# Kernel optimization log

Measured on AMD Instinct MI355X. Metric: run time of the kernel, lower is better.

The kernel has to match this reference:

```python
import jax, jax.numpy as jnp
import numpy as np

B, C, H, W = 4, 512, 64, 64
D = 512  # model_dim


def setup_inputs() -> dict:
    key = jax.random.key(0)
    ks = jax.random.split(key, 9)
    s = 0.02
    return {
        "q": jax.random.normal(ks[0], (B, C, H, W), dtype=jnp.float32),
        "Wq": jax.random.normal(ks[1], (D, C), dtype=jnp.float32) * s,
        "bq": jax.random.normal(ks[2], (D,), dtype=jnp.float32) * s,
        "Wk": jax.random.normal(ks[3], (D, C), dtype=jnp.float32) * s,
        "bk": jax.random.normal(ks[4], (D,), dtype=jnp.float32) * s,
        "Wv": jax.random.normal(ks[5], (D, C), dtype=jnp.float32) * s,
        "bv": jax.random.normal(ks[6], (D,), dtype=jnp.float32) * s,
        "Wo": jax.random.normal(ks[7], (C, D), dtype=jnp.float32) * s,
        "bo": jax.random.normal(ks[8], (C,), dtype=jnp.float32) * s,
    }


def reference(q, Wq, bq, Wk, bk, Wv, bv, Wo, bo):
    b, c, h, w = q.shape
    # 1x1 conv == per-pixel linear over channels; tokens s = h*w
    x = q.reshape(b, c, h * w)                      # (b, c, s)
    Q = jnp.einsum('bcs,dc->bsd', x, Wq) + bq       # (b, s, D)
    K = jnp.einsum('bcs,dc->bsd', x, Wk) + bk
    V = jnp.einsum('bcs,dc->bsd', x, Wv) + bv
    # ScaleAttend: scale = q.shape[-1]^-0.5 = model_dim^-0.5 (heads not split)
    scale = jnp.asarray(Q.shape[-1], Q.dtype) ** -0.5
    sim = jnp.einsum('bsd,btd->bst', Q, K) * scale  # (b, s, s)
    attn = jax.nn.softmax(sim, axis=-1)
    o = jnp.einsum('bst,btd->bsd', attn, V)         # (b, s, D)
    # to_out 1x1 conv: D -> C
    y = jnp.einsum('bsd,cd->bsc', o, Wo) + bo       # (b, s, C)
    return y.transpose(0, 2, 1).reshape(b, c, h, w)
```

## Files before the change

### kernel.cpp

```cpp
#include <hip/hip_runtime.h>
#include <hip/hip_bf16.h>

typedef __hip_bfloat16 bf16;
typedef __attribute__((ext_vector_type(8))) short short8;
typedef __attribute__((ext_vector_type(4))) float floatx4;
typedef __attribute__((ext_vector_type(4))) short shortx4;

static constexpr int BATCH = 4;
static constexpr int CH    = 512;
static constexpr int SEQ   = 4096;
static constexpr int DM    = 512;

__device__ __forceinline__ void gload16(const void* g, void* l) {
  __builtin_amdgcn_global_load_lds(
      (const __attribute__((address_space(1))) unsigned int*)g,
      (__attribute__((address_space(3))) unsigned int*)l,
      16, 0, 0);
}

__device__ __forceinline__ float hw_exp2(float x) {
  float r;
  asm("v_exp_f32 %0, %1" : "=v"(r) : "v"(x));
  return r;
}

__global__ __launch_bounds__(256) void cvt_weights(
    const float* __restrict__ w0, const float* __restrict__ w1,
    const float* __restrict__ w2, const float* __restrict__ w3,
    bf16* __restrict__ out) {
  const float* src = (blockIdx.y == 0) ? w0 : (blockIdx.y == 1) ? w1
                   : (blockIdx.y == 2) ? w2 : w3;
  int idx = blockIdx.x * 256 + threadIdx.x;
  out[(long)blockIdx.y * (DM * CH) + idx] = __float2bfloat16(src[idx]);
}

__global__ __launch_bounds__(256) void transpose_cvt(
    const float* __restrict__ x, bf16* __restrict__ xT) {
  __shared__ float tile[64][65];
  const int s0 = blockIdx.x * 64, c0 = blockIdx.y * 64;
  const float* xb = x + (long)blockIdx.z * CH * SEQ;
  bf16* xTb = xT + (long)blockIdx.z * SEQ * CH;
  const int t = threadIdx.x;
  const int sl = t & 63, cq = t >> 6;
  #pragma unroll
  for (int i = 0; i < 16; ++i) {
    int cl = cq * 16 + i;
    tile[cl][sl] = xb[(long)(c0 + cl) * SEQ + s0 + sl];
  }
  __syncthreads();
  const int cl2 = t & 63, sq = t >> 6;
  #pragma unroll
  for (int i = 0; i < 16; ++i) {
    int sl2 = sq * 16 + i;
    xTb[(long)(s0 + sl2) * CH + c0 + cl2] = __float2bfloat16(tile[cl2][sl2]);
  }
}

template <int KIND>
__global__ __launch_bounds__(256, 2) void proj128(
    const bf16* __restrict__ A0, const bf16* __restrict__ Wbase,
    const float* __restrict__ b0, const float* __restrict__ b1,
    const float* __restrict__ b2, void* __restrict__ Cbase) {
  __shared__ __align__(16) bf16 As[2][128 * 64];
  __shared__ __align__(16) bf16 Bs[2][128 * 64];

  int id = blockIdx.x + gridDim.x * (blockIdx.y + gridDim.y * blockIdx.z);
  int nwg = gridDim.x * gridDim.y * gridDim.z;
  int sid = ((nwg & 7) == 0) ? ((id & 7) * (nwg >> 3) + (id >> 3)) : id;
  const int bx = sid % gridDim.x;
  const int by = (sid / gridDim.x) % gridDim.y;
  const int z  = sid / (gridDim.x * gridDim.y);
  const int mat = (KIND == 0) ? (z >> 2) : 0;
  const int bz  = (KIND == 0) ? (z & 3) : z;

  const long XSZ = (long)SEQ * CH;
  const long lK = CH;
  const bf16* Ab = A0 + (long)bz * XSZ + (long)by * 128 * lK;
  const bf16* Bb = Wbase + (long)mat * ((long)DM * CH) + (long)bx * 128 * lK;
  const float* bias = (KIND == 1) ? b0 : (mat == 0 ? b0 : mat == 1 ? b1 : b2);

  const int tid = threadIdx.x;
  const int w = tid >> 6, lane = tid & 63;
  const int wr = w >> 1, wc = w & 1;
  const int l16 = lane & 15, quad = lane >> 4;
  const int srow = tid >> 3;
  const int sp = tid & 7;
  const int slog = (sp ^ (srow & 7)) << 3;
  const int pA0 = (quad ^ (l16 & 7)) << 3;
  const int pA1 = pA0 ^ 32;

  auto stageA = [&](int buf, int kt) {
    const bf16* s = Ab + kt * 64 + (long)srow * lK + slog;
    char* d = (char*)(&As[buf][0]) + tid * 16;
    #pragma unroll
    for (int r = 0; r < 4; ++r)
      gload16(s + (long)(r * 32) * lK, d + r * 4096);
  };
  auto stageB = [&](int buf, int kt) {
    const bf16* s = Bb + kt * 64 + (long)srow * lK + slog;
    char* d = (char*)(&Bs[buf][0]) + tid * 16;
    #pragma unroll
    for (int r = 0; r < 4; ++r)
      gload16(s + (long)(r * 32) * lK, d + r * 4096);
  };

  floatx4 acc[4][4];
  #pragma unroll
  for (int m = 0; m < 4; ++m)
    #pragma unroll
    for (int n = 0; n < 4; ++n) acc[m][n] = (floatx4)(0.0f);

  const int nk = CH >> 6;
  stageA(0, 0); stageB(0, 0);
  __syncthreads();

  for (int t = 0; t < nk; ++t) {
    const int cur = t & 1, nxt = cur ^ 1;
    const bool more = (t + 1 < nk);
    #pragma unroll
    for (int kc = 0; kc < 2; ++kc) {
      const int poff = kc ? pA1 : pA0;
      short8 a[4], b[4];
      #pragma unroll
      for (int i = 0; i < 4; ++i)
        a[i] = *(const short8*)(&As[cur][0] + (wr * 64 + i * 16 + l16) * 64 + poff);
      #pragma unroll
      for (int j = 0; j < 4; ++j)
        b[j] = *(const short8*)(&Bs[cur][0] + (wc * 64 + j * 16 + l16) * 64 + poff);
      if (more) {
        if (kc == 0) stageA(nxt, t + 1);
        else         stageB(nxt, t + 1);
      }
      __builtin_amdgcn_s_setprio(1);
      #pragma unroll
      for (int i = 0; i < 4; ++i)
        #pragma unroll
        for (int j = 0; j < 4; ++j)
          acc[i][j] = __builtin_amdgcn_mfma_f32_16x16x32_bf16(
              a[i], b[j], acc[i][j], 0, 0, 0);
      __builtin_amdgcn_s_setprio(0);
    }
    __syncthreads();
  }

  const int rbase = by * 128 + wr * 64 + quad * 4;
  const int cbase = bx * 128 + wc * 64 + l16;
  #pragma unroll
  for (int m = 0; m < 4; ++m) {
    const int row = rbase + m * 16;
    #pragma unroll
    for (int n = 0; n < 4; ++n) {
      const int col = cbase + n * 16;
      floatx4 v = acc[m][n];
      const float bb = bias[col];
      if constexpr (KIND == 0) {
        if (mat < 2) {
          bf16* C = (bf16*)Cbase + (long)mat * (BATCH * XSZ) + (long)bz * XSZ;
          #pragma unroll
          for (int r = 0; r < 4; ++r)
            C[(long)(row + r) * DM + col] = __float2bfloat16(v[r] + bb);
        } else {
          bf16* C = (bf16*)Cbase + 2 * (BATCH * XSZ) + (long)bz * XSZ;
          alignas(8) bf16 tmp[4];
          #pragma unroll
          for (int r = 0; r < 4; ++r) tmp[r] = __float2bfloat16(v[r] + bb);
          *(shortx4*)(C + (long)col * SEQ + row) = *(const shortx4*)tmp;
        }
      } else {
        float* C = (float*)Cbase + (long)bz * XSZ;
        floatx4 o_;
        #pragma unroll
        for (int r = 0; r < 4; ++r) o_[r] = v[r] + bb;
        *(floatx4*)(C + (long)col * SEQ + row) = o_;
      }
    }
  }
}

__global__ __launch_bounds__(512, 2) void gemm_qk(
    const bf16* __restrict__ A, long sAz,
    const bf16* __restrict__ B, long sBz,
    bf16* __restrict__ C, long sCz,
    float scale, int K, int ldc) {
  __shared__ __align__(16) bf16 As[2][256 * 64];
  __shared__ __align__(16) bf16 Bs[2][256 * 64];

  int id = blockIdx.x + gridDim.x * (blockIdx.y + gridDim.y * blockIdx.z);
  int nwg = gridDim.x * gridDim.y * gridDim.z;
  int sid = ((nwg & 7) == 0) ? ((id & 7) * (nwg >> 3) + (id >> 3)) : id;
  const int bx = sid % gridDim.x;
  const int by = (sid / gridDim.x) % gridDim.y;
  const int bz = sid / (gridDim.x * gridDim.y);

  const int tid = threadIdx.x;
  const long lK = K;
  const bf16* Ab = A + (long)bz * sAz + (long)by * 256 * lK;
  const bf16* Bb = B + (long)bz * sBz + (long)bx * 256 * lK;

  const int w = tid >> 6, lane = tid & 63;
  const int wr = w >> 2, wc = w & 3;
  const int l16 = lane & 15, quad = lane >> 4;

  const int srow = tid >> 3;
  const int sp = tid & 7;
  const int slog = (sp ^ (srow & 7)) << 3;

  const int pA0 = (quad ^ (l16 & 7)) << 3;
  const int pA1 = pA0 ^ 32;

  auto stage_half = [&](const bf16* Gb, bf16* Lb, int kt, int h) {
    #pragma unroll
    for (int r = 0; r < 2; ++r) {
      const int row = h * 128 + r * 64 + srow;
      gload16(Gb + (long)kt * 64 + (long)row * lK + slog,
              (char*)Lb + row * 128 + sp * 16);
    }
  };

  floatx4 acc[8][4];
  #pragma unroll
  for (int m = 0; m < 8; ++m)
    #pragma unroll
    for (int n = 0; n < 4; ++n) acc[m][n] = (floatx4)(0.0f);

  const int nk = K >> 6;
  stage_half(Ab, &As[0][0], 0, 0); stage_half(Bb, &Bs[0][0], 0, 0);
  stage_half(Ab, &As[0][0], 0, 1); stage_half(Bb, &Bs[0][0], 0, 1);
  if (nk > 1) { stage_half(Ab, &As[1][0], 1, 0); stage_half(Bb, &Bs[1][0], 1, 0); }
  asm volatile("s_waitcnt vmcnt(4)" ::: "memory");
  __builtin_amdgcn_s_barrier();

  for (int tt = 0; tt < nk; tt += 2) {
    #pragma unroll
    for (int u = 0; u < 2; ++u) {
      const bf16* __restrict__ Al = &As[u][0];
      const bf16* __restrict__ Bl = &Bs[u][0];
      short8 a[2][4], b[2][2][2];
      #pragma unroll
      for (int p = 0; p < 4; ++p) {
        const int rm = p >> 1, cn = p & 1;
        if (cn == 0) {
          #pragma unroll
          for (int kc = 0; kc < 2; ++kc)
            #pragma unroll
            for (int i = 0; i < 4; ++i)
              a[kc][i] = *(const short8*)(
                  Al + (rm * 128 + wr * 64 + i * 16 + l16) * 64
                     + (kc ? pA1 : pA0));
        }
        if (rm == 0) {
          #pragma unroll
          for (int kc = 0; kc < 2; ++kc)
            #pragma unroll
            for (int j = 0; j < 2; ++j)
              b[kc][cn][j] = *(const short8*)(
                  Bl + (cn * 128 + wc * 32 + j * 16 + l16) * 64
                     + (kc ? pA1 : pA0));
        }
        {
          const int g = u * 4 + p;
          const int stile = tt + 1 + ((g + 2) >> 2);
          if (stile < nk) {
            const int sh = (p < 2) ? 1 : 0;
            if (p & 1) stage_half(Bb, &Bs[stile & 1][0], stile, sh);
            else       stage_half(Ab, &As[stile & 1][0], stile, sh);
          }
        }
        __builtin_amdgcn_sched_barrier(0);
        __builtin_amdgcn_s_barrier();
        asm volatile("s_waitcnt lgkmcnt(0)" ::: "memory");
        __builtin_amdgcn_sched_barrier(0);
        __builtin_amdgcn_s_setprio(1);
        #pragma unroll
        for (int kc = 0; kc < 2; ++kc)
          #pragma unroll
          for (int i = 0; i < 4; ++i)
            #pragma unroll
            for (int j = 0; j < 2; ++j)
              acc[rm * 4 + i][cn * 2 + j] =
                  __builtin_amdgcn_mfma_f32_16x16x32_bf16(
                      a[kc][i], b[kc][cn][j], acc[rm * 4 + i][cn * 2 + j],
                      0, 0, 0);
        __builtin_amdgcn_s_setprio(0);
        if (p == 3) {
          if (u == 0) {
            if (tt + 2 < nk) asm volatile("s_waitcnt vmcnt(4)" ::: "memory");
            else             asm volatile("s_waitcnt vmcnt(0)" ::: "memory");
          } else {
            if (tt + 2 < nk) asm volatile("s_waitcnt vmcnt(4)" ::: "memory");
          }
        }
        __builtin_amdgcn_s_barrier();
      }
    }
  }

  bf16* Cb = C + (long)bz * sCz;
  #pragma unroll
  for (int rm = 0; rm < 2; ++rm)
    #pragma unroll
    for (int i = 0; i < 4; ++i) {
      const int row = by * 256 + rm * 128 + wr * 64 + i * 16 + quad * 4;
      #pragma unroll
      for (int cn = 0; cn < 2; ++cn)
        #pragma unroll
        for (int j = 0; j < 2; ++j) {
          const int col = bx * 256 + cn * 128 + wc * 32 + j * 16 + l16;
          floatx4 v = acc[rm * 4 + i][cn * 2 + j];
          #pragma unroll
          for (int r = 0; r < 4; ++r)
            Cb[(long)(row + r) * ldc + col] = __float2bfloat16(v[r] * scale);
        }
    }
}

__global__ __launch_bounds__(512, 2) void fused_smpv(
    const bf16* __restrict__ Sim, const bf16* __restrict__ Vt,
    bf16* __restrict__ Ob) {
  __shared__ __align__(16) bf16 Apv[2][64 * 64];
  __shared__ float rl_lds[64];

  const int id = blockIdx.x + (blockIdx.y << 6);
  const int xcd = id & 7;
  const int bz = xcd >> 1;
  const int by = ((id >> 3) << 1) | (id & 1);

  const int tid = threadIdx.x;
  const bf16* Simb = Sim + (long)bz * ((long)SEQ * SEQ) + (long)(by * 64) * SEQ;
  const bf16* Vb   = Vt  + (long)bz * ((long)SEQ * CH);
  bf16* Obb        = Ob  + (long)bz * ((long)SEQ * CH) + (long)(by * 64) * CH;

  const int srow = tid >> 3;
  const int sp = tid & 7;
  const int aswz = (sp ^ (srow & 7)) << 4;

  const int w = tid >> 6, lane = tid & 63;
  const int l16 = lane & 15, quad = lane >> 4;
  const int pA0 = (quad ^ (l16 & 7)) << 3;
  const int pA1 = pA0 ^ 32;

  const bf16* Vw = Vb + (long)(w * 64 + l16) * SEQ + quad * 8;

  float lsum = 0.f;

  auto writeA = [&](int buf, uint4 u) {
    const ushort* h = (const ushort*)&u;
    union { uint4 u4; ushort hh[8]; } pk;
    #pragma unroll
    for (int k2 = 0; k2 < 8; ++k2) {
      float f = __uint_as_float(((unsigned)h[k2]) << 16);
      float e = hw_exp2(f);
      lsum += e;
      __hip_bfloat16 pb = __float2bfloat16(e);
      pk.hh[k2] = *(const ushort*)&pb;
    }
    *(uint4*)((char*)(&Apv[buf][0]) + srow * 128 + aswz) = pk.u4;
  };

  {
    uint4 ua = *(const uint4*)(Simb + (long)srow * SEQ + sp * 8);
    writeA(0, ua);
  }
  __syncthreads();

  floatx4 acc[4][4];
  #pragma unroll
  for (int i = 0; i < 4; ++i)
    #pragma unroll
    for (int j = 0; j < 4; ++j) acc[i][j] = (floatx4)(0.0f);

  const int nk = SEQ >> 6;
  for (int t = 0; t < nk; ++t) {
    const int cur = t & 1, nxt = cur ^ 1;
    const bool more = (t + 1 < nk);
    short8 b[2][4];
    #pragma unroll
    for (int j = 0; j < 4; ++j) {
      const bf16* p = Vw + (long)(j * 16) * SEQ + t * 64;
      b[0][j] = *(const short8*)(p);
      b[1][j] = *(const short8*)(p + 32);
    }
    uint4 un;
    if (more)
      un = *(const uint4*)(Simb + (long)srow * SEQ + (t + 1) * 64 + sp * 8);
    short8 a[2][4];
    #pragma unroll
    for (int kc = 0; kc < 2; ++kc) {
      const int poff = kc ? pA1 : pA0;
      #pragma unroll
      for (int i = 0; i < 4; ++i)
        a[kc][i] = *(const short8*)(&Apv[cur][0] + (i * 16 + l16) * 64 + poff);
    }
    __builtin_amdgcn_s_setprio(1);
    #pragma unroll
    for (int kc = 0; kc < 2; ++kc)
      #pragma unroll
      for (int i = 0; i < 4; ++i)
        #pragma unroll
        for (int j = 0; j < 4; ++j)
          acc[i][j] = __builtin_amdgcn_mfma_f32_16x16x32_bf16(
              a[kc][i], b[kc][j], acc[i][j], 0, 0, 0);
    __builtin_amdgcn_s_setprio(0);
    if (more) writeA(nxt, un);
    __syncthreads();
  }

  #pragma unroll
  for (int o = 1; o < 8; o <<= 1) lsum += __shfl_xor(lsum, o);
  if (sp == 0) rl_lds[srow] = 1.0f / lsum;
  __syncthreads();

  #pragma unroll
  for (int i = 0; i < 4; ++i) {
    #pragma unroll
    for (int j = 0; j < 4; ++j) {
      floatx4 v = acc[i][j];
      const int col = w * 64 + j * 16 + l16;
      #pragma unroll
      for (int r = 0; r < 4; ++r) {
        const int row = i * 16 + quad * 4 + r;
        Obb[(long)row * CH + col] = __float2bfloat16(v[r] * rl_lds[row]);
      }
    }
  }
}

extern "C" void kernel_launch(void* const* d_in, const int* in_sizes, int n_in,
                              void* d_out, int out_size, void* d_ws,
                              size_t ws_size, hipStream_t stream) {
  const float* q  = (const float*)d_in[0];
  const float* Wq = (const float*)d_in[1];
  const float* bq = (const float*)d_in[2];
  const float* Wk = (const float*)d_in[3];
  const float* bk = (const float*)d_in[4];
  const float* Wv = (const float*)d_in[5];
  const float* bv = (const float*)d_in[6];
  const float* Wo = (const float*)d_in[7];
  const float* bo = (const float*)d_in[8];
  float* out = (float*)d_out;

  bf16* ws = (bf16*)d_ws;
  const long WSZ = (long)DM * CH;
  const long XSZ = (long)SEQ * CH;
  const long SSZ = (long)SEQ * SEQ;
  bf16* Wqb = ws;
  bf16* Wob = Wqb + 3 * WSZ;
  bf16* xT  = Wqb + 4 * WSZ;
  bf16* Qb  = xT + BATCH * XSZ;
  bf16* Kb  = Qb + BATCH * XSZ;
  bf16* Vt  = Kb + BATCH * XSZ;
  bf16* Ob  = Vt + BATCH * XSZ;
  bf16* Sim = Ob + BATCH * XSZ;

  cvt_weights<<<dim3(WSZ / 256, 4), 256, 0, stream>>>(Wq, Wk, Wv, Wo, ws);
  transpose_cvt<<<dim3(SEQ / 64, CH / 64, BATCH), 256, 0, stream>>>(q, xT);

  proj128<0><<<dim3(4, 32, 12), 256, 0, stream>>>(
      xT, Wqb, bq, bk, bv, Qb);
  const float qkscale = 0.04419417382415922f * 1.4426950408889634f;
  gemm_qk<<<dim3(16, 16, BATCH), 512, 0, stream>>>(
      Qb, XSZ, Kb, XSZ, Sim, SSZ, qkscale, CH, SEQ);
  fused_smpv<<<dim3(64, 4), 512, 0, stream>>>(Sim, Vt, Ob);
  proj128<1><<<dim3(4, 32, 4), 256, 0, stream>>>(
      Ob, Wob, bo, nullptr, nullptr, out);
}
```

Baseline: 405.4 us.

## Register double-buffer V tiles and unroll PV loop by two with lighter barriers

Unrolls the P·V accumulation loop by two and keeps two register sets of V fragments, so the global loads for the next tile are issued a full iteration before the MFMAs that consume them. The previous version loaded V at the top of each iteration and then waited on it. __syncthreads is replaced by an explicit lgkmcnt wait, s_barrier and sched_barrier, which avoids waiting on outstanding global (vmcnt) loads at the barrier. The cost is higher VGPR pressure from the extra short8 buffers, which could lower occupancy or cause spills.

```diff
diff --git a/kernel.cpp b/kernel.cpp
--- a/kernel.cpp
+++ b/kernel.cpp
@@ -357,11 +357,24 @@
     *(uint4*)((char*)(&Apv[buf][0]) + srow * 128 + aswz) = pk.u4;
   };
 
+  short8 bA[2][4], bB[2][4];
+  auto loadV = [&](short8 (&dst)[2][4], int t) {
+    #pragma unroll
+    for (int j = 0; j < 4; ++j) {
+      const bf16* p = Vw + (long)(j * 16) * SEQ + t * 64;
+      dst[0][j] = *(const short8*)(p);
+      dst[1][j] = *(const short8*)(p + 32);
+    }
+  };
+
   {
     uint4 ua = *(const uint4*)(Simb + (long)srow * SEQ + sp * 8);
+    loadV(bA, 0);
     writeA(0, ua);
   }
-  __syncthreads();
+  asm volatile("s_waitcnt lgkmcnt(0)" ::: "memory");
+  __builtin_amdgcn_s_barrier();
+  __builtin_amdgcn_sched_barrier(0);
 
   floatx4 acc[4][4];
   #pragma unroll
@@ -370,39 +383,65 @@
     for (int j = 0; j < 4; ++j) acc[i][j] = (floatx4)(0.0f);
 
   const int nk = SEQ >> 6;
-  for (int t = 0; t < nk; ++t) {
-    const int cur = t & 1, nxt = cur ^ 1;
-    const bool more = (t + 1 < nk);
-    short8 b[2][4];
-    #pragma unroll
-    for (int j = 0; j < 4; ++j) {
-      const bf16* p = Vw + (long)(j * 16) * SEQ + t * 64;
-      b[0][j] = *(const short8*)(p);
-      b[1][j] = *(const short8*)(p + 32);
-    }
-    uint4 un;
-    if (more)
-      un = *(const uint4*)(Simb + (long)srow * SEQ + (t + 1) * 64 + sp * 8);
-    short8 a[2][4];
-    #pragma unroll
-    for (int kc = 0; kc < 2; ++kc) {
-      const int poff = kc ? pA1 : pA0;
-      #pragma unroll
-      for (int i = 0; i < 4; ++i)
-        a[kc][i] = *(const short8*)(&Apv[cur][0] + (i * 16 + l16) * 64 + poff);
-    }
-    __builtin_amdgcn_s_setprio(1);
-    #pragma unroll
-    for (int kc = 0; kc < 2; ++kc)
-      #pragma unroll
-      for (int i = 0; i < 4; ++i)
-        #pragma unroll
-        for (int j = 0; j < 4; ++j)
-          acc[i][j] = __builtin_amdgcn_mfma_f32_16x16x32_bf16(
-              a[kc][i], b[kc][j], acc[i][j], 0, 0, 0);
-    __builtin_amdgcn_s_setprio(0);
-    if (more) writeA(nxt, un);
-    __syncthreads();
+  for (int t = 0; t < nk; t += 2) {
+    {
+      loadV(bB, t + 1);
+      uint4 un = *(const uint4*)(Simb + (long)srow * SEQ + (t + 1) * 64 + sp * 8);
+      short8 a[2][4];
+      #pragma unroll
+      for (int kc = 0; kc < 2; ++kc) {
+        const int poff = kc ? pA1 : pA0;
+        #pragma unroll
+        for (int i = 0; i < 4; ++i)
+          a[kc][i] = *(const short8*)(&Apv[0][0] + (i * 16 + l16) * 64 + poff);
+      }
+      __builtin_amdgcn_s_setprio(1);
+      #pragma unroll
+      for (int kc = 0; kc < 2; ++kc)
+        #pragma unroll
+        for (int i = 0; i < 4; ++i)
+          #pragma unroll
+          for (int j = 0; j < 4; ++j)
+            acc[i][j] = __builtin_amdgcn_mfma_f32_16x16x32_bf16(
+                a[kc][i], bA[kc][j], acc[i][j], 0, 0, 0);
+      __builtin_amdgcn_s_setprio(0);
+      writeA(1, un);
+      asm volatile("s_waitcnt lgkmcnt(0)" ::: "memory");
+      __builtin_amdgcn_s_barrier();
+      __builtin_amdgcn_sched_barrier(0);
+    }
+    {
+      const bool more = (t + 2 < nk);
+      uint4 un2;
+      if (more) {
+        loadV(bA, t + 2);
+        un2 = *(const uint4*)(Simb + (long)srow * SEQ + (t + 2) * 64 + sp * 8);
+      }
+      short8 a[2][4];
+      #pragma unroll
+      for (int kc = 0; kc < 2; ++kc) {
+        const int poff = kc ? pA1 : pA0;
+        #pragma unroll
+        for (int i = 0; i < 4; ++i)
+          a[kc][i] = *(const short8*)(&Apv[1][0] + (i * 16 + l16) * 64 + poff);
+      }
+      __builtin_amdgcn_s_setprio(1);
+      #pragma unroll
+      for (int kc = 0; kc < 2; ++kc)
+        #pragma unroll
+        for (int i = 0; i < 4; ++i)
+          #pragma unroll
+          for (int j = 0; j < 4; ++j)
+            acc[i][j] = __builtin_amdgcn_mfma_f32_16x16x32_bf16(
+                a[kc][i], bB[kc][j], acc[i][j], 0, 0, 0);
+      __builtin_amdgcn_s_setprio(0);
+      if (more) {
+        writeA(0, un2);
+        asm volatile("s_waitcnt lgkmcnt(0)" ::: "memory");
+        __builtin_amdgcn_s_barrier();
+        __builtin_amdgcn_sched_barrier(0);
+      }
+    }
   }
 
   #pragma unroll
```

Measured after the change: 396.8 us. -2.1%, faster.
